# Kernel tuning notes

Hardware: AMD Instinct MI355X
Metric: run time of the kernel (lower is better)

## Reference

```python
import jax, jax.numpy as jnp
import numpy as np

B, N, C = 8, 1024, 768
H = 12
HD = C // H
R = 16  # LoRA rank
SCALE = HD ** -0.5


def setup_inputs() -> dict:
    key = jax.random.key(0)
    ks = jax.random.split(key, 13)
    s = C ** -0.5
    return {
        "x": jax.random.normal(ks[0], (B, N, C), jnp.float32),
        "Wq": jax.random.normal(ks[1], (C, C), jnp.float32) * s,
        "Wk": jax.random.normal(ks[2], (C, C), jnp.float32) * s,
        "Wv": jax.random.normal(ks[3], (C, C), jnp.float32) * s,
        "Wp": jax.random.normal(ks[4], (C, C), jnp.float32) * s,
        "bp": jax.random.normal(ks[5], (C,), jnp.float32) * 0.02,
        "la_q": jax.random.normal(ks[6], (C, R), jnp.float32) * s,
        "lb_q": jax.random.normal(ks[7], (R, C), jnp.float32) * (R ** -0.5),
        "la_k": jax.random.normal(ks[8], (C, R), jnp.float32) * s,
        "lb_k": jax.random.normal(ks[9], (R, C), jnp.float32) * (R ** -0.5),
        "la_v": jax.random.normal(ks[10], (C, R), jnp.float32) * s,
        "lb_v": jax.random.normal(ks[11], (R, C), jnp.float32) * (R ** -0.5),
        "block_weight": jax.random.uniform(ks[12], (3,), jnp.float32),
    }


def _split_heads(t):
    # [B, N, C] -> [B, H, N, HD]
    return t.reshape(B, N, H, HD).transpose(0, 2, 1, 3)


def reference(x, Wq, Wk, Wv, Wp, bp, la_q, lb_q, la_k, lb_k, la_v, lb_v, block_weight):
    # q/k/v projections (qkv_bias=False) + LoRA adapter injection (msa=[1,1,1])
    q = x @ Wq + block_weight[0] * ((x @ la_q) @ lb_q)
    k = x @ Wk + block_weight[1] * ((x @ la_k) @ lb_k)
    v = x @ Wv + block_weight[2] * ((x @ la_v) @ lb_v)

    qh = _split_heads(q)  # [B,H,N,HD]
    kh = _split_heads(k)
    vh = _split_heads(v)

    # full NxN scores, scale, softmax (attn_drop=0 -> identity)
    attn = jnp.einsum("bhnd,bhmd->bhnm", qh, kh) * SCALE
    attn = jax.nn.softmax(attn, axis=-1)
    out = jnp.einsum("bhnm,bhmd->bhnd", attn, vh)  # [B,H,N,HD]
    out = out.transpose(0, 2, 1, 3).reshape(B, N, C)

    # output projection (proj_drop=0 -> identity)
    return out @ Wp + bp
```

## Files before the change

kernel.cpp:

```cpp
#include <hip/hip_runtime.h>

#define BB 8
#define NN 1024
#define CC 768
#define HH 12
#define HD 64
#define RR 16
#define MM (BB * NN)
#define WSZ (CC * CC)
#define NT (NN / 64)

#define KSC 0.18033688011112042f

typedef short bf16x8 __attribute__((ext_vector_type(8)));
typedef short bf16x4 __attribute__((ext_vector_type(4)));
typedef float f32x4 __attribute__((ext_vector_type(4)));

__device__ __forceinline__ unsigned short f2bf(float f) {
    unsigned u = __builtin_bit_cast(unsigned, f);
    unsigned r = (u + 0x7FFFu + ((u >> 16) & 1u)) >> 16;
    return (unsigned short)r;
}
__device__ __forceinline__ float bf2f(unsigned short s) {
    return __builtin_bit_cast(float, ((unsigned)s) << 16);
}

__device__ __forceinline__ float fast_exp2(float x) {
#if __has_builtin(__builtin_amdgcn_exp2f)
    return __builtin_amdgcn_exp2f(x);
#else
    return exp2f(x);
#endif
}

__device__ __forceinline__ unsigned cvt_pk_bf16(float a, float b) {
    unsigned r;
    asm("v_cvt_pk_bf16_f32 %0, %1, %2" : "=v"(r) : "v"(a), "v"(b));
    return r;
}

__device__ __forceinline__ void gload16(const void* g, void* l) {
    __builtin_amdgcn_global_load_lds(
        (const __attribute__((address_space(1))) unsigned int*)g,
        (__attribute__((address_space(3))) unsigned int*)l, 16, 0, 0);
}

__device__ __forceinline__ void wait_vm0_barrier() {
    asm volatile("s_waitcnt vmcnt(0)" ::: "memory");
    __builtin_amdgcn_s_barrier();
}

__global__ __launch_bounds__(256) void prep_w(
    const float* __restrict__ Wq, const float* __restrict__ Wk,
    const float* __restrict__ Wv, const float* __restrict__ Wp,
    const float* __restrict__ la_q, const float* __restrict__ lb_q,
    const float* __restrict__ la_k, const float* __restrict__ lb_k,
    const float* __restrict__ la_v, const float* __restrict__ lb_v,
    const float* __restrict__ bw, short* __restrict__ wt_hi,
    short* __restrict__ wt_lo) {
    __shared__ float laS[64][16];
    __shared__ float lbS[16][64];
    __shared__ float T[64][65];

    const int z = blockIdx.z;
    const int k0 = blockIdx.y * 64, n0 = blockIdx.x * 64;
    const int tid = threadIdx.x;

    const float* W = (z == 0) ? Wq : (z == 1) ? Wk : (z == 2) ? Wv : Wp;
    const float* la = (z == 0) ? la_q : (z == 1) ? la_k : la_v;
    const float* lb = (z == 0) ? lb_q : (z == 1) ? lb_k : lb_v;
    const float bwz = (z < 3) ? bw[z] : 0.f;

    if (z < 3) {
        #pragma unroll
        for (int e = 0; e < 4; ++e) {
            int idx = tid + 256 * e;
            laS[idx >> 4][idx & 15] = la[(size_t)(k0 + (idx >> 4)) * RR + (idx & 15)];
            lbS[idx >> 6][idx & 63] = lb[(size_t)(idx >> 6) * CC + n0 + (idx & 63)];
        }
    }
    __syncthreads();

    #pragma unroll
    for (int e = 0; e < 16; ++e) {
        int idx = tid + 256 * e;
        int row = idx >> 6, col = idx & 63;
        float v = W[(size_t)(k0 + row) * CC + n0 + col];
        if (z < 3) {
            float s = 0.f;
            #pragma unroll
            for (int r = 0; r < 16; ++r) s += laS[row][r] * lbS[r][col];
            v += bwz * s;
        }
        T[row][col] = v;
    }
    __syncthreads();

    short* oh = wt_hi + (size_t)z * WSZ;
    short* ol = wt_lo + (size_t)z * WSZ;
    #pragma unroll
    for (int e = 0; e < 16; ++e) {
        int idx = tid + 256 * e;
        int nrow = idx >> 6, kcol = idx & 63;
        float v = T[kcol][nrow];
        unsigned short hi = f2bf(v);
        unsigned short lo = f2bf(v - bf2f(hi));
        size_t off = (size_t)(n0 + nrow) * CC + k0 + kcol;
        oh[off] = (short)hi;
        ol[off] = (short)lo;
    }
}

__global__ __launch_bounds__(256) void prep_cvt(const float* __restrict__ src,
                                                short* __restrict__ hi, int n4) {
    int i = blockIdx.x * 256 + threadIdx.x;
    const int stride = gridDim.x * 256;
    for (; i < n4; i += stride) {
        f32x4 v = ((const f32x4*)src)[i];
        bf16x4 h;
        #pragma unroll
        for (int c = 0; c < 4; ++c) h[c] = (short)f2bf(v[c]);
        ((bf16x4*)hi)[i] = h;
    }
}

__device__ __forceinline__ void stage_plain(const short* __restrict__ gA,
                                            const short* __restrict__ gB,
                                            int rowA0, int rowB0, int kt,
                                            short* Lb, int tid) {
    const int fr = ((tid >> 6) << 4) | (tid & 15);
    const int kc = ((tid >> 4) & 3) * 8 + kt;
    const size_t ga0 = (size_t)(rowA0 + fr) * CC + kc;
    const size_t gb0 = (size_t)(rowB0 + fr) * CC + kc;
    short* d0 = Lb + tid * 8;
    short* d1 = Lb + (tid + 256) * 8;
    gload16(gA + ga0, d0);
    gload16(gA + ga0 + (size_t)64 * CC, d1);
    gload16(gB + gb0, d0 + 4096);
    gload16(gB + gb0 + (size_t)64 * CC, d1 + 4096);
}

__device__ __forceinline__ void gemm_core_plain(const short* __restrict__ gA,
                                                int rowA0,
                                                const short* __restrict__ gB,
                                                int rowB0, short (*L)[8192],
                                                f32x4 acc[4][4]) {
    const int tid = threadIdx.x, lane = tid & 63, w = tid >> 6;
    const int wm = w >> 1, wn = w & 1;
    stage_plain(gA, gB, rowA0, rowB0, 0, L[0], tid);
    for (int ki = 0; ki < 24; ++ki) {
        wait_vm0_barrier();
        if (ki < 23)
            stage_plain(gA, gB, rowA0, rowB0, (ki + 1) * 32, L[(ki + 1) & 1],
                        tid);
        const short* Lb = L[ki & 1];
        bf16x8 ah[4], bh[4];
        #pragma unroll
        for (int i = 0; i < 4; ++i)
            ah[i] = *(const bf16x8*)(Lb + (wm * 4 + i) * 512 + lane * 8);
        #pragma unroll
        for (int j = 0; j < 4; ++j)
            bh[j] = *(const bf16x8*)(Lb + 4096 + (wn * 4 + j) * 512 + lane * 8);
        #pragma unroll
        for (int i = 0; i < 4; ++i)
            #pragma unroll
            for (int j = 0; j < 4; ++j)
                acc[i][j] = __builtin_amdgcn_mfma_f32_16x16x32_bf16(
                    ah[i], bh[j], acc[i][j], 0, 0, 0);
    }
}

__global__ __launch_bounds__(256, 4) void gemm_qkv(
    const short* __restrict__ xh, const short* __restrict__ wth,
    short* __restrict__ qb, short* __restrict__ kb, short* __restrict__ vtb) {
    __shared__ __align__(16) short L[2][8192];

    int flat = blockIdx.x + 6 * blockIdx.y + 384 * blockIdx.z;
    int swz = (flat & 7) * 144 + (flat >> 3);
    int z = swz / 384;
    int rem = swz - z * 384;
    int by = rem / 6, bx = rem - by * 6;
    const int m0 = by * 128, c0 = bx * 128;

    const short* wzh = wth + (size_t)z * WSZ;

    f32x4 acc[4][4];
    const f32x4 z4 = {0.f, 0.f, 0.f, 0.f};
    #pragma unroll
    for (int i = 0; i < 4; ++i)
        #pragma unroll
        for (int j = 0; j < 4; ++j) acc[i][j] = z4;

    const int lane = threadIdx.x & 63, w = threadIdx.x >> 6;
    const int wm = w >> 1, wn = w & 1, p = lane & 15, g = lane >> 4;

    if (z < 2) {
        gemm_core_plain(xh, m0, wzh, c0, L, acc);
        short* dst = (z == 0) ? qb : kb;
        const float scl = (z == 0) ? KSC : 1.0f;
        #pragma unroll
        for (int i = 0; i < 4; ++i) {
            #pragma unroll
            for (int r = 0; r < 4; ++r) {
                int m = m0 + wm * 64 + i * 16 + 4 * g + r;
                int b = m >> 10, n = m & 1023;
                #pragma unroll
                for (int j = 0; j < 4; ++j) {
                    int c = c0 + wn * 64 + j * 16 + p;
                    int h = c >> 6, d = c & 63;
                    dst[(((size_t)(b * HH + h)) * NN + n) * HD + d] =
                        (short)f2bf(acc[i][j][r] * scl);
                }
            }
        }
    } else {
        gemm_core_plain(wzh, c0, xh, m0, L, acc);
        #pragma unroll
        for (int i = 0; i < 4; ++i) {
            #pragma unroll
            for (int r = 0; r < 4; ++r) {
                int c = c0 + wm * 64 + i * 16 + 4 * g + r;
                int h = c >> 6, d = c & 63;
                #pragma unroll
                for (int j = 0; j < 4; ++j) {
                    int m = m0 + wn * 64 + j * 16 + p;
                    int b = m >> 10, n = m & 1023;
                    vtb[(((size_t)(b * HH + h)) * HD + d) * NN + n] =
                        (short)f2bf(acc[i][j][r]);
                }
            }
        }
    }
}

__device__ __forceinline__ void stage_kv(const short* __restrict__ kp,
                                         const short* __restrict__ vp, int j0,
                                         short* Kd, short* Vd, int tid) {
    const int pp = tid & 15;
    const int kc = ((tid >> 4) & 3) * 8 + ((tid >> 6) & 1) * 32;
    const int r0 = tid >> 7;
    gload16(kp + (size_t)(j0 + r0 * 16 + pp) * HD + kc, Kd + tid * 8);
    gload16(kp + (size_t)(j0 + (r0 + 2) * 16 + pp) * HD + kc, Kd + (tid + 256) * 8);
    gload16(vp + (size_t)(r0 * 16 + pp) * NN + j0 + kc, Vd + tid * 8);
    gload16(vp + (size_t)((r0 + 2) * 16 + pp) * NN + j0 + kc, Vd + (tid + 256) * 8);
}

__global__ __launch_bounds__(256, 4) void attn(const short* __restrict__ qb,
                                               const short* __restrict__ kb,
                                               const short* __restrict__ vtb,
                                               short* __restrict__ aoh,
                                               short* __restrict__ aol) {
    __shared__ __align__(16) short QP[4096];
    __shared__ __align__(16) short Kb[2][4096];
    __shared__ __align__(16) short Vb[2][4096];

    int flat = blockIdx.x + 16 * blockIdx.y;
    int swz = (flat & 7) * 192 + (flat >> 3);
    const int q0 = (swz & 15) * 64;
    const int bh = swz >> 4;

    const int tid = threadIdx.x, lane = tid & 63, w = tid >> 6;
    const int p = lane & 15, g = lane >> 4;
    const short* qp = qb + (size_t)bh * NN * HD;
    const short* kp = kb + (size_t)bh * NN * HD;
    const short* vp = vtb + (size_t)bh * NN * HD;

    {
        const int kc = ((tid >> 4) & 3) * 8 + ((tid >> 6) & 1) * 32;
        const int r0 = tid >> 7;
        gload16(qp + (size_t)(q0 + r0 * 16 + p) * HD + kc, QP + tid * 8);
        gload16(qp + (size_t)(q0 + (r0 + 2) * 16 + p) * HD + kc,
                QP + (tid + 256) * 8);
    }
    stage_kv(kp, vp, 0, Kb[0], Vb[0], tid);
    wait_vm0_barrier();

    bf16x8 bQ[2];
    bQ[0] = *(const bf16x8*)(QP + (w * 2 + 0) * 512 + lane * 8);
    bQ[1] = *(const bf16x8*)(QP + (w * 2 + 1) * 512 + lane * 8);

    float m_run = -1e30f, l_run = 0.f;
    f32x4 oacc[4];
    const f32x4 z4 = {0.f, 0.f, 0.f, 0.f};
    #pragma unroll
    for (int df = 0; df < 4; ++df) oacc[df] = z4;
    short* Pw = QP + w * 1024;

    for (int t = 0; t < NT; ++t) {
        if (t) wait_vm0_barrier();
        if (t < NT - 1)
            stage_kv(kp, vp, (t + 1) * 64, Kb[(t + 1) & 1], Vb[(t + 1) & 1], tid);
        const short* Kc = Kb[t & 1];
        const short* Vc = Vb[t & 1];

        f32x4 sacc[4];
        #pragma unroll
        for (int jf = 0; jf < 4; ++jf) sacc[jf] = z4;
        #pragma unroll
        for (int ks = 0; ks < 2; ++ks) {
            #pragma unroll
            for (int jf = 0; jf < 4; ++jf) {
                bf16x8 aK =
                    *(const bf16x8*)(Kc + jf * 1024 + ks * 512 + lane * 8);
                sacc[jf] = __builtin_amdgcn_mfma_f32_16x16x32_bf16(
                    aK, bQ[ks], sacc[jf], 0, 0, 0);
            }
        }

        float tmax = sacc[0][0];
        #pragma unroll
        for (int jf = 0; jf < 4; ++jf)
            #pragma unroll
            for (int r = 0; r < 4; ++r) tmax = fmaxf(tmax, sacc[jf][r]);
        tmax = fmaxf(tmax, __shfl_xor(tmax, 16));
        tmax = fmaxf(tmax, __shfl_xor(tmax, 32));
        if (__any(tmax > m_run + 3.0f)) {
            const float mnew = fmaxf(m_run, tmax);
            const float fac = fast_exp2(m_run - mnew);
            m_run = mnew;
            l_run *= fac;
            #pragma unroll
            for (int r = 0; r < 4; ++r) {
                float fr = __shfl(fac, 4 * g + r, 16);
                #pragma unroll
                for (int df = 0; df < 4; ++df) oacc[df][r] *= fr;
            }
        }
        float lsum = 0.f;
        #pragma unroll
        for (int jf = 0; jf < 4; ++jf) {
            #pragma unroll
            for (int r = 0; r < 4; ++r) {
                float e = fast_exp2(sacc[jf][r] - m_run);
                sacc[jf][r] = e;
                lsum += e;
            }
        }
        lsum += __shfl_xor(lsum, 16);
        lsum += __shfl_xor(lsum, 32);
        l_run += lsum;

        #pragma unroll
        for (int jf = 0; jf < 4; ++jf) {
            uint2 wpk;
            wpk.x = cvt_pk_bf16(sacc[jf][0], sacc[jf][1]);
            wpk.y = cvt_pk_bf16(sacc[jf][2], sacc[jf][3]);
            *(uint2*)(Pw + (jf >> 1) * 512 +
                      (((jf & 1) * 2 + (g >> 1)) * 16 + p) * 8 + (g & 1) * 4) =
                wpk;
        }
        asm volatile("s_waitcnt lgkmcnt(0)" ::: "memory");
        __builtin_amdgcn_sched_barrier(0);

        #pragma unroll
        for (int ks = 0; ks < 2; ++ks) {
            bf16x8 aP = *(const bf16x8*)(Pw + ks * 512 + lane * 8);
            #pragma unroll
            for (int df = 0; df < 4; ++df) {
                bf16x8 bV =
                    *(const bf16x8*)(Vc + df * 1024 + ks * 512 + lane * 8);
                oacc[df] = __builtin_amdgcn_mfma_f32_16x16x32_bf16(
                    aP, bV, oacc[df], 0, 0, 0);
            }
        }
    }

    const float inv = 1.f / l_run;
    const int b = bh / HH, h = bh % HH;
    #pragma unroll
    for (int r = 0; r < 4; ++r) {
        float ir = __shfl(inv, 4 * g + r, 16);
        int n = q0 + w * 16 + 4 * g + r;
        #pragma unroll
        for (int df = 0; df < 4; ++df) {
            float v = oacc[df][r] * ir;
            unsigned short hi = f2bf(v);
            unsigned short lo = f2bf(v - bf2f(hi));
            size_t off = ((size_t)(b * NN + n)) * CC + h * HD + df * 16 + p;
            aoh[off] = (short)hi;
            aol[off] = (short)lo;
        }
    }
}

__device__ __forceinline__ void stage_split(const short* __restrict__ gAh,
                                            const short* __restrict__ gAl,
                                            const short* __restrict__ gBh,
                                            const short* __restrict__ gBl,
                                            int rowA0, int rowB0, int kt,
                                            short* Lb, int tid) {
    const int fr = ((tid >> 6) << 4) | (tid & 15);
    const int kc = ((tid >> 4) & 3) * 8 + kt;
    const size_t ga0 = (size_t)(rowA0 + fr) * CC + kc;
    const size_t ga1 = ga0 + (size_t)64 * CC;
    const size_t gb0 = (size_t)(rowB0 + fr) * CC + kc;
    const size_t gb1 = gb0 + (size_t)64 * CC;
    short* d0 = Lb + tid * 8;
    short* d1 = Lb + (tid + 256) * 8;
    gload16(gAh + ga0, d0);
    gload16(gAh + ga1, d1);
    gload16(gAl + ga0, d0 + 4096);
    gload16(gAl + ga1, d1 + 4096);
    gload16(gBh + gb0, d0 + 8192);
    gload16(gBh + gb1, d1 + 8192);
    gload16(gBl + gb0, d0 + 12288);
    gload16(gBl + gb1, d1 + 12288);
}

__global__ __launch_bounds__(256, 2) void gemm_proj(
    const short* __restrict__ aoh, const short* __restrict__ aol,
    const short* __restrict__ wth, const short* __restrict__ wtl,
    const float* __restrict__ bp, float* __restrict__ out) {
    __shared__ __align__(16) short L[2][4 * 4096];

    int flat = blockIdx.x + 6 * blockIdx.y;
    int swz = (flat & 7) * 48 + (flat >> 3);
    int by = swz / 6, bx = swz - by * 6;
    const int m0 = by * 128, c0 = bx * 128;

    const short* wph = wth + (size_t)3 * WSZ;
    const short* wpl = wtl + (size_t)3 * WSZ;

    f32x4 acc[4][4];
    const f32x4 z4 = {0.f, 0.f, 0.f, 0.f};
    #pragma unroll
    for (int i = 0; i < 4; ++i)
        #pragma unroll
        for (int j = 0; j < 4; ++j) acc[i][j] = z4;

    const int tid = threadIdx.x, lane = tid & 63, w = tid >> 6;
    const int wm = w >> 1, wn = w & 1, p = lane & 15, g = lane >> 4;

    stage_split(aoh, aol, wph, wpl, m0, c0, 0, L[0], tid);
    for (int ki = 0; ki < 24; ++ki) {
        wait_vm0_barrier();
        if (ki < 23)
            stage_split(aoh, aol, wph, wpl, m0, c0, (ki + 1) * 32,
                        L[(ki + 1) & 1], tid);
        const short* Lb = L[ki & 1];
        const int fb = lane * 8;
        bf16x8 ah[4], al[4], bh[4], bl[4];
        #pragma unroll
        for (int i = 0; i < 4; ++i) {
            ah[i] = *(const bf16x8*)(Lb + (wm * 4 + i) * 512 + fb);
            al[i] = *(const bf16x8*)(Lb + 4096 + (wm * 4 + i) * 512 + fb);
        }
        #pragma unroll
        for (int j = 0; j < 4; ++j) {
            bh[j] = *(const bf16x8*)(Lb + 8192 + (wn * 4 + j) * 512 + fb);
            bl[j] = *(const bf16x8*)(Lb + 12288 + (wn * 4 + j) * 512 + fb);
        }
        #pragma unroll
        for (int i = 0; i < 4; ++i) {
            #pragma unroll
            for (int j = 0; j < 4; ++j) {
                acc[i][j] = __builtin_amdgcn_mfma_f32_16x16x32_bf16(
                    ah[i], bh[j], acc[i][j], 0, 0, 0);
                acc[i][j] = __builtin_amdgcn_mfma_f32_16x16x32_bf16(
                    ah[i], bl[j], acc[i][j], 0, 0, 0);
                acc[i][j] = __builtin_amdgcn_mfma_f32_16x16x32_bf16(
                    al[i], bh[j], acc[i][j], 0, 0, 0);
            }
        }
    }

    float bpv[4];
    #pragma unroll
    for (int j = 0; j < 4; ++j) bpv[j] = bp[c0 + wn * 64 + j * 16 + p];

    #pragma unroll
    for (int i = 0; i < 4; ++i) {
        #pragma unroll
        for (int r = 0; r < 4; ++r) {
            int m = m0 + wm * 64 + i * 16 + 4 * g + r;
            #pragma unroll
            for (int j = 0; j < 4; ++j) {
                int c = c0 + wn * 64 + j * 16 + p;
                out[(size_t)m * CC + c] = acc[i][j][r] + bpv[j];
            }
        }
    }
}

extern "C" void kernel_launch(void* const* d_in, const int* in_sizes, int n_in,
                              void* d_out, int out_size, void* d_ws,
                              size_t ws_size, hipStream_t stream) {
    const float* x = (const float*)d_in[0];
    const float* Wq = (const float*)d_in[1];
    const float* Wk = (const float*)d_in[2];
    const float* Wv = (const float*)d_in[3];
    const float* Wp = (const float*)d_in[4];
    const float* bp = (const float*)d_in[5];
    const float* la_q = (const float*)d_in[6];
    const float* lb_q = (const float*)d_in[7];
    const float* la_k = (const float*)d_in[8];
    const float* lb_k = (const float*)d_in[9];
    const float* la_v = (const float*)d_in[10];
    const float* lb_v = (const float*)d_in[11];
    const float* bw = (const float*)d_in[12];
    float* out = (float*)d_out;

    short* ws = (short*)d_ws;
    short* wt_hi = ws;
    short* wt_lo = wt_hi + (size_t)4 * WSZ;
    short* x_hi = wt_lo + (size_t)4 * WSZ;
    short* qbuf = x_hi + (size_t)MM * CC;
    short* kbuf = qbuf + (size_t)MM * CC;
    short* vtbuf = kbuf + (size_t)MM * CC;
    short* aoh = vtbuf + (size_t)MM * CC;
    short* aol = aoh + (size_t)MM * CC;

    prep_w<<<dim3(CC / 64, CC / 64, 4), 256, 0, stream>>>(
        Wq, Wk, Wv, Wp, la_q, lb_q, la_k, lb_k, la_v, lb_v, bw, wt_hi, wt_lo);
    prep_cvt<<<2048, 256, 0, stream>>>(x, x_hi, MM * CC / 4);
    gemm_qkv<<<dim3(CC / 128, MM / 128, 3), 256, 0, stream>>>(
        x_hi, wt_hi, qbuf, kbuf, vtbuf);
    attn<<<dim3(NN / 64, BB * HH), 256, 0, stream>>>(qbuf, kbuf, vtbuf, aoh, aol);
    gemm_proj<<<dim3(CC / 128, MM / 128), 256, 0, stream>>>(aoh, aol, wt_hi,
                                                            wt_lo, bp, out);
}
```

Before: 274.6 us.

## Fuse Q, K, V projections into one GEMM sharing x tiles, transpose V via LDS

Replaces the three separate per-projection GEMM blocks with a single kernel where each block computes Q, K and V tiles for the same 128x128 output region. Each x tile is loaded once and reused across all three weight matrices, cutting global traffic for x. The V output is transposed through shared memory so it can be written with vectorized row stores instead of scattered 2-byte stores. The block now holds 48 accumulator vectors and uses double the LDS, lowering occupancy to 2 blocks per CU and reducing the grid to 384 blocks.

New measurement: 266.8 us. -2.9%, faster.

```diff
diff --git a/kernel.cpp b/kernel.cpp
--- a/kernel.cpp
+++ b/kernel.cpp
@@ -124,80 +124,79 @@
     }
 }
 
-__device__ __forceinline__ void stage_plain(const short* __restrict__ gA,
-                                            const short* __restrict__ gB,
-                                            int rowA0, int rowB0, int kt,
-                                            short* Lb, int tid) {
+__device__ __forceinline__ void stage_fused(const short* __restrict__ xh,
+                                            const short* __restrict__ wth,
+                                            int m0, int c0, int kt, short* Lb,
+                                            int tid) {
     const int fr = ((tid >> 6) << 4) | (tid & 15);
     const int kc = ((tid >> 4) & 3) * 8 + kt;
-    const size_t ga0 = (size_t)(rowA0 + fr) * CC + kc;
-    const size_t gb0 = (size_t)(rowB0 + fr) * CC + kc;
+    const size_t ga = (size_t)(m0 + fr) * CC + kc;
+    const size_t gw = (size_t)(c0 + fr) * CC + kc;
     short* d0 = Lb + tid * 8;
     short* d1 = Lb + (tid + 256) * 8;
-    gload16(gA + ga0, d0);
-    gload16(gA + ga0 + (size_t)64 * CC, d1);
-    gload16(gB + gb0, d0 + 4096);
-    gload16(gB + gb0 + (size_t)64 * CC, d1 + 4096);
-}
-
-__device__ __forceinline__ void gemm_core_plain(const short* __restrict__ gA,
-                                                int rowA0,
-                                                const short* __restrict__ gB,
-                                                int rowB0, short (*L)[8192],
-                                                f32x4 acc[4][4]) {
+    gload16(xh + ga, d0);
+    gload16(xh + ga + (size_t)64 * CC, d1);
+    gload16(wth + gw, d0 + 4096);
+    gload16(wth + gw + (size_t)64 * CC, d1 + 4096);
+    gload16(wth + WSZ + gw, d0 + 8192);
+    gload16(wth + WSZ + gw + (size_t)64 * CC, d1 + 8192);
+    gload16(wth + 2 * (size_t)WSZ + gw, d0 + 12288);
+    gload16(wth + 2 * (size_t)WSZ + gw + (size_t)64 * CC, d1 + 12288);
+}
+
+__global__ __launch_bounds__(256, 2) void gemm_qkv_fused(
+    const short* __restrict__ xh, const short* __restrict__ wth,
+    short* __restrict__ qb, short* __restrict__ kb, short* __restrict__ vtb) {
+    __shared__ __align__(16) short L[2][16384];
+
+    int flat = blockIdx.x + 6 * blockIdx.y;
+    int swz = (flat & 7) * 48 + (flat >> 3);
+    int by = swz / 6, bx = swz - by * 6;
+    const int m0 = by * 128, c0 = bx * 128;
+
     const int tid = threadIdx.x, lane = tid & 63, w = tid >> 6;
-    const int wm = w >> 1, wn = w & 1;
-    stage_plain(gA, gB, rowA0, rowB0, 0, L[0], tid);
+    const int wm = w >> 1, wn = w & 1, p = lane & 15, g = lane >> 4;
+
+    f32x4 acc[3][4][4];
+    const f32x4 z4 = {0.f, 0.f, 0.f, 0.f};
+    #pragma unroll
+    for (int z = 0; z < 3; ++z)
+        #pragma unroll
+        for (int i = 0; i < 4; ++i)
+            #pragma unroll
+            for (int j = 0; j < 4; ++j) acc[z][i][j] = z4;
+
+    stage_fused(xh, wth, m0, c0, 0, L[0], tid);
     for (int ki = 0; ki < 24; ++ki) {
         wait_vm0_barrier();
         if (ki < 23)
-            stage_plain(gA, gB, rowA0, rowB0, (ki + 1) * 32, L[(ki + 1) & 1],
+            stage_fused(xh, wth, m0, c0, (ki + 1) * 32, L[(ki + 1) & 1],
                         tid);
         const short* Lb = L[ki & 1];
-        bf16x8 ah[4], bh[4];
+        bf16x8 ah[4];
         #pragma unroll
         for (int i = 0; i < 4; ++i)
             ah[i] = *(const bf16x8*)(Lb + (wm * 4 + i) * 512 + lane * 8);
         #pragma unroll
-        for (int j = 0; j < 4; ++j)
-            bh[j] = *(const bf16x8*)(Lb + 4096 + (wn * 4 + j) * 512 + lane * 8);
-        #pragma unroll
-        for (int i = 0; i < 4; ++i)
+        for (int z = 0; z < 3; ++z) {
+            const short* Bz = Lb + 4096 * (z + 1);
+            bf16x8 bh[4];
             #pragma unroll
             for (int j = 0; j < 4; ++j)
-                acc[i][j] = __builtin_amdgcn_mfma_f32_16x16x32_bf16(
-                    ah[i], bh[j], acc[i][j], 0, 0, 0);
-    }
-}
-
-__global__ __launch_bounds__(256, 4) void gemm_qkv(
-    const short* __restrict__ xh, const short* __restrict__ wth,
-    short* __restrict__ qb, short* __restrict__ kb, short* __restrict__ vtb) {
-    __shared__ __align__(16) short L[2][8192];
-
-    int flat = blockIdx.x + 6 * blockIdx.y + 384 * blockIdx.z;
-    int swz = (flat & 7) * 144 + (flat >> 3);
-    int z = swz / 384;
-    int rem = swz - z * 384;
-    int by = rem / 6, bx = rem - by * 6;
-    const int m0 = by * 128, c0 = bx * 128;
-
-    const short* wzh = wth + (size_t)z * WSZ;
-
-    f32x4 acc[4][4];
-    const f32x4 z4 = {0.f, 0.f, 0.f, 0.f};
-    #pragma unroll
-    for (int i = 0; i < 4; ++i)
-        #pragma unroll
-        for (int j = 0; j < 4; ++j) acc[i][j] = z4;
-
-    const int lane = threadIdx.x & 63, w = threadIdx.x >> 6;
-    const int wm = w >> 1, wn = w & 1, p = lane & 15, g = lane >> 4;
-
-    if (z < 2) {
-        gemm_core_plain(xh, m0, wzh, c0, L, acc);
-        short* dst = (z == 0) ? qb : kb;
-        const float scl = (z == 0) ? KSC : 1.0f;
+                bh[j] = *(const bf16x8*)(Bz + (wn * 4 + j) * 512 + lane * 8);
+            #pragma unroll
+            for (int i = 0; i < 4; ++i)
+                #pragma unroll
+                for (int j = 0; j < 4; ++j)
+                    acc[z][i][j] = __builtin_amdgcn_mfma_f32_16x16x32_bf16(
+                        ah[i], bh[j], acc[z][i][j], 0, 0, 0);
+        }
+    }
+
+    #pragma unroll
+    for (int zz = 0; zz < 2; ++zz) {
+        short* dst = (zz == 0) ? qb : kb;
+        const float scl = (zz == 0) ? KSC : 1.0f;
         #pragma unroll
         for (int i = 0; i < 4; ++i) {
             #pragma unroll
@@ -209,27 +208,37 @@
                     int c = c0 + wn * 64 + j * 16 + p;
                     int h = c >> 6, d = c & 63;
                     dst[(((size_t)(b * HH + h)) * NN + n) * HD + d] =
-                        (short)f2bf(acc[i][j][r] * scl);
+                        (short)f2bf(acc[zz][i][j][r] * scl);
                 }
             }
         }
-    } else {
-        gemm_core_plain(wzh, c0, xh, m0, L, acc);
-        #pragma unroll
-        for (int i = 0; i < 4; ++i) {
-            #pragma unroll
-            for (int r = 0; r < 4; ++r) {
-                int c = c0 + wm * 64 + i * 16 + 4 * g + r;
-                int h = c >> 6, d = c & 63;
-                #pragma unroll
-                for (int j = 0; j < 4; ++j) {
-                    int m = m0 + wn * 64 + j * 16 + p;
-                    int b = m >> 10, n = m & 1023;
-                    vtb[(((size_t)(b * HH + h)) * HD + d) * NN + n] =
-                        (short)f2bf(acc[i][j][r]);
-                }
-            }
-        }
+    }
+
+    __syncthreads();
+    short* Lt = &L[0][0];
+    #pragma unroll
+    for (int i = 0; i < 4; ++i) {
+        #pragma unroll
+        for (int r = 0; r < 4; ++r) {
+            int mp = wm * 64 + i * 16 + 4 * g + r;
+            #pragma unroll
+            for (int j = 0; j < 4; ++j) {
+                int cp = wn * 64 + j * 16 + p;
+                Lt[cp * 132 + mp] = (short)f2bf(acc[2][i][j][r]);
+            }
+        }
+    }
+    __syncthreads();
+    {
+        const int cp = tid >> 1, mh = (tid & 1) * 64;
+        const int c = c0 + cp, h = c >> 6, d = c & 63;
+        const int b = m0 >> 10, nbase = m0 & 1023;
+        short* dst =
+            vtb + ((size_t)(b * HH + h) * HD + d) * NN + nbase + mh;
+        #pragma unroll
+        for (int e = 0; e < 16; ++e)
+            *(bf16x4*)(dst + e * 4) =
+                *(const bf16x4*)(Lt + cp * 132 + mh + e * 4);
     }
 }
 
@@ -513,7 +522,7 @@
     prep_w<<<dim3(CC / 64, CC / 64, 4), 256, 0, stream>>>(
         Wq, Wk, Wv, Wp, la_q, lb_q, la_k, lb_k, la_v, lb_v, bw, wt_hi, wt_lo);
     prep_cvt<<<2048, 256, 0, stream>>>(x, x_hi, MM * CC / 4);
-    gemm_qkv<<<dim3(CC / 128, MM / 128, 3), 256, 0, stream>>>(
+    gemm_qkv_fused<<<dim3(CC / 128, MM / 128), 256, 0, stream>>>(
         x_hi, wt_hi, qbuf, kbuf, vtbuf);
     attn<<<dim3(NN / 64, BB * HH), 256, 0, stream>>>(qbuf, kbuf, vtbuf, aoh, aol);
     gemm_proj<<<dim3(CC / 128, MM / 128), 256, 0, stream>>>(aoh, aol, wt_hi,
```
